# Performance work log

Measured on AMD Instinct MI355X. Metric: run time of the kernel, lower is better.

## Reference

```python
import jax, jax.numpy as jnp
import numpy as np

B, N, OBS, H, HEADS = 8192, 32, 128, 256, 4
HD = H // HEADS  # head dim = 64
GAIN = (0.125 / H) ** 0.5
LN_EPS = 1e-5


def _ln(x):
    # LayerNorm over last dim, no affine (elementwise_affine=False)
    m = x.mean(axis=-1, keepdims=True)
    v = ((x - m) ** 2).mean(axis=-1, keepdims=True)
    return (x - m) * jax.lax.rsqrt(v + LN_EPS)


def setup_inputs() -> dict:
    key = jax.random.key(0)
    ks = jax.random.split(key, 20)
    f32 = jnp.float32
    # weights stored (in, out) so y = x @ W + b (transpose of torch layout)
    def w(k, i, o, g):
        return (jax.random.normal(k, (i, o), dtype=f32) * g)
    inp = {
        "all_agent_obs": jax.random.normal(ks[0], (B, N, OBS), dtype=f32),
        # EntityEmbedding (obs-only): 1-layer LinearEncoder, normal init * t-fixup gain
        "W_emb": w(ks[1], OBS, H, GAIN), "b_emb": jnp.zeros((H,), f32),
        # ResidualSelfAttention projections
        "Wq": w(ks[2], H, H, GAIN), "bq": jnp.zeros((H,), f32),
        "Wk": w(ks[3], H, H, GAIN), "bk": jnp.zeros((H,), f32),
        "Wv": w(ks[4], H, H, GAIN), "bv": jnp.zeros((H,), f32),
        "Wo": w(ks[5], H, H, GAIN), "bo": jnp.zeros((H,), f32),
        # LinearEncoder tail (num_layers=2), kaiming-ish scale * t-fixup gain
        "W1": w(ks[6], H, H, GAIN), "b1": jnp.zeros((H,), f32),
        "W2": w(ks[7], H, H, GAIN), "b2": jnp.zeros((H,), f32),
        # value head: Linear(h_size + 1, 1)
        "Wval": w(ks[8], H + 1, 1, (1.0 / (H + 1)) ** 0.5), "bval": jnp.zeros((1,), f32),
    }
    return inp


def reference(all_agent_obs, W_emb, b_emb, Wq, bq, Wk, bk, Wv, bv, Wo, bo,
              W1, b1, W2, b2, Wval, bval):
    # --- EntityEmbedding: 1-layer MLP with SiLU ---
    ent = jax.nn.silu(jnp.einsum("bno,oh->bnh", all_agent_obs, W_emb) + b_emb)

    # --- ResidualSelfAttention (pre-norm, no mask) ---
    x = _ln(ent)                                        # embedding_norm
    q = (x @ Wq + bq).reshape(B, N, HEADS, HD)
    k = (x @ Wk + bk).reshape(B, N, HEADS, HD)
    v = (x @ Wv + bv).reshape(B, N, HEADS, HD)
    attn = jnp.einsum("bnhd,bmhd->bhnm", q, k) / jnp.sqrt(jnp.float32(HD))
    attn = jax.nn.softmax(attn, axis=-1)
    out = jnp.einsum("bhnm,bmhd->bnhd", attn, v).reshape(B, N, H)
    out = _ln(out @ Wo + bo + x)                        # fc_out + residual, residual_norm
    pooled = out.mean(axis=1)                           # (B, H) unmasked avg pool

    # --- LinearEncoder tail (2 layers, SiLU) ---
    enc = jax.nn.silu(pooled @ W1 + b1)
    enc = jax.nn.silu(enc @ W2 + b2)

    # --- norm agent count: max_agents updates to N, so val = N*2/N - 1 = 1.0 ---
    nc = jnp.ones((B, 1), dtype=enc.dtype)
    enc = jnp.concatenate([enc, nc], axis=-1)           # (B, H+1)
    return enc @ Wval + bval                            # (B, 1)
```

## Files before the change

### kernel.cpp

```cpp
#include <hip/hip_runtime.h>


typedef __bf16 bf16x8 __attribute__((ext_vector_type(8)));
typedef float f32x4 __attribute__((ext_vector_type(4)));
typedef unsigned short ushort_t;

#define DEVI static __device__ __forceinline__
#define MFMA16(a, b, cc) __builtin_amdgcn_mfma_f32_16x16x32_bf16((a), (b), (cc), 0, 0, 0)

#define WAITV2 asm volatile("s_waitcnt vmcnt(2)" ::: "memory")
#define WAITV0 asm volatile("s_waitcnt vmcnt(0)" ::: "memory")
#define WAITLG asm volatile("s_waitcnt lgkmcnt(0)" ::: "memory")
#define BAR() __builtin_amdgcn_s_barrier()

constexpr int OWemb_ = 0;
constexpr int OWq_   = 32768;
constexpr int OWk_   = OWq_ + 65536;
constexpr int OWv_   = OWk_ + 65536;
constexpr int OWo_   = OWv_ + 65536;
constexpr int OW1_   = OWo_ + 65536;
constexpr int OW2_   = OW1_ + 65536;

constexpr int OBS_STRIDE = 264;
constexpr int L_BST = 32768;
constexpr int L_PP  = 65536;
constexpr int LDS_TOTAL = 65536 + 2048;
static_assert(LDS_TOTAL <= 80 * 1024, "need <=80KB for 2 blocks/CU");

DEVI float silu_f(float x) { return x / (1.0f + __expf(-x)); }
DEVI f32x4 splat4(float x) { f32x4 v = {x, x, x, x}; return v; }
DEVI uint2 pack4(f32x4 v) {
  union { __bf16 h[4]; uint2 u; } x;
  x.h[0] = (__bf16)v[0]; x.h[1] = (__bf16)v[1];
  x.h[2] = (__bf16)v[2]; x.h[3] = (__bf16)v[3];
  return x.u;
}
DEVI f32x4 unpk(uint2 u) {
  union { uint2 u2; __bf16 h[4]; } x; x.u2 = u;
  f32x4 v = {(float)x.h[0], (float)x.h[1], (float)x.h[2], (float)x.h[3]};
  return v;
}
DEVI bf16x8 ld_frag(const char* p) { return *(const bf16x8*)p; }
DEVI bf16x8 u4b(unsigned a, unsigned b, unsigned cc, unsigned d) {
  union { unsigned u[4]; bf16x8 v; } x;
  x.u[0] = a; x.u[1] = b; x.u[2] = cc; x.u[3] = d;
  return x.v;
}
DEVI unsigned to_agpr(unsigned v) {
  unsigned d;
  asm volatile("v_accvgpr_write_b32 %0, %1" : "=a"(d) : "v"(v));
  return d;
}
DEVI unsigned from_agpr(unsigned a) {
  unsigned d;
  asm volatile("v_accvgpr_read_b32 %0, %1" : "=v"(d) : "a"(a));
  return d;
}
DEVI int xaddr(int row, int k4) {
  int t = row >> 4, cc = row & 15;
  int ks = k4 >> 5, kg = (k4 >> 3) & 3, half = (k4 >> 2) & 1;
  return ((t * 8 + ks) * 64 + kg * 16 + cc) * 16 + half * 8;
}

typedef const __attribute__((address_space(1))) unsigned int* gas_ptr;
typedef __attribute__((address_space(3))) unsigned int* las_ptr;
DEVI void gload16(const void* g, void* l) {
  __builtin_amdgcn_global_load_lds((gas_ptr)g, (las_ptr)l, 16, 0, 0);
}

constexpr int CSRC(int p) {
  return (p < 4)  ? (OWemb_ + p * 8192)
       : (p < 12) ? (OWq_ + (p - 4) * 8192)
       : (p < 20) ? (OWk_ + (p - 12) * 8192)
       : (p < 28) ? (OWv_ + (p - 20) * 8192)
                  : (OWo_ + (p - 28) * 8192);
}

DEVI void issue_chunk(const ushort_t* pw, int srcOff, char* bst, int slot, int wv, int lane) {
  char* dst = bst + slot * 16384 + wv * 2048;
  const ushort_t* s = pw + srcOff + wv * 1024 + (size_t)lane * 8;
  gload16(s, dst);
  gload16(s + 512, dst + 1024);
}
#define PH_ISSUE(p) issue_chunk(pw, CSRC(p), bst, (p) & 1, wv, lane)

__global__ void pack_weights(const float* __restrict__ Wemb, const float* __restrict__ Wq,
                             const float* __restrict__ Wk, const float* __restrict__ Wv,
                             const float* __restrict__ Wo, const float* __restrict__ W1,
                             const float* __restrict__ W2, ushort_t* __restrict__ ws) {
  int t = blockIdx.x * 256 + threadIdx.x;
  if (t >= 53248) return;
  const float* src;
  int dst, n, k0;
  if (t < 4096) {
    int rem = t & 1023;
    int ctg = rem >> 6, l = rem & 63;
    n = ctg * 16 + (l & 15);
    k0 = (t >> 10) * 32 + (l >> 4) * 8;
    src = Wemb; dst = OWemb_ + t * 8;
  } else if (t < 36864) {
    int u = t - 4096, m = u >> 13, loc = u & 8191;
    int rem = loc & 1023;
    int ctg = rem >> 6, l = rem & 63;
    n = ctg * 16 + (l & 15);
    k0 = (loc >> 10) * 32 + (l >> 4) * 8;
    src = (m == 0) ? Wq : (m == 1) ? Wk : (m == 2) ? Wv : Wo;
    dst = OWq_ + m * 65536 + loc * 8;
  } else {
    int u = t - 36864, m = u >> 13, loc = u & 8191;
    int ln = loc & 63, ks = (loc >> 6) & 7, ct = loc >> 9;
    n = ct * 16 + (ln & 15);
    k0 = ks * 32 + (ln >> 4) * 8;
    src = m ? W2 : W1; dst = OW1_ + m * 65536 + loc * 8;
  }
  union { __bf16 h[8]; uint4 u; } pk;
  #pragma unroll
  for (int j = 0; j < 8; ++j) pk.h[j] = (__bf16)src[(k0 + j) * 256 + n];
  *(uint4*)(ws + dst) = pk.u;
}

__global__ __launch_bounds__(512, 4)
void poca_fused(const float* __restrict__ obs, const ushort_t* __restrict__ pw,
                const float* __restrict__ b_emb, const float* __restrict__ bq,
                const float* __restrict__ bk, const float* __restrict__ bv,
                const float* __restrict__ bo, const float* __restrict__ b1,
                const float* __restrict__ b2, const float* __restrict__ Wval,
                const float* __restrict__ bval, float* __restrict__ out) {
  __shared__ __align__(128) char lds[LDS_TOTAL];
  const int tid = threadIdx.x;
  const int wv = tid >> 6, lane = tid & 63;
  const int g = lane >> 4, c = lane & 15;
  const int mg = wv >> 2, ng = wv & 3;
  char* xb = lds;
  char* bst = lds + L_BST;
  char* as_ = bst + wv * 4096;
  char* ppb = lds + L_PP;
  char* poolb = bst;
  char* y1b = bst + 8448;
  char* ptlb = bst + 16896;

  PH_ISSUE(0);

  {
    const float4* op = (const float4*)(obs + (size_t)blockIdx.x * 64 * 128);
    #pragma unroll
    for (int it = 0; it < 4; ++it) {
      int idx = it * 512 + tid;
      float4 v = op[idx];
      int row = idx >> 5, col4 = idx & 31;
      union { __bf16 h[4]; uint2 u; } cv;
      cv.h[0] = (__bf16)v.x; cv.h[1] = (__bf16)v.y;
      cv.h[2] = (__bf16)v.z; cv.h[3] = (__bf16)v.w;
      *(uint2*)(xb + row * OBS_STRIDE + col4 * 8) = cv.u;
    }
  }
  WAITLG;

  f32x4 acc[2][4];

  #pragma unroll
  for (int p = 0; p < 4; ++p) {
    PH_ISSUE(p + 1); WAITV2; BAR();
    if (p == 0) {
      #pragma unroll
      for (int ct = 0; ct < 4; ++ct) {
        f32x4 b_ = *(const f32x4*)(b_emb + ng * 64 + ct * 16 + g * 4);
        acc[0][ct] = b_; acc[1][ct] = b_;
      }
    }
    const char* ck = bst + (p & 1) * 16384;
    bf16x8 wf[4], xf[2];
    #pragma unroll
    for (int t = 0; t < 4; ++t) wf[t] = ld_frag(ck + ((ng * 4 + t) * 64 + lane) * 16);
    #pragma unroll
    for (int rt = 0; rt < 2; ++rt)
      xf[rt] = ld_frag(xb + ((mg * 2 + rt) * 16 + c) * OBS_STRIDE + p * 64 + g * 16);
    #pragma unroll
    for (int rt = 0; rt < 2; ++rt)
      #pragma unroll
      for (int ct = 0; ct < 4; ++ct) acc[rt][ct] = MFMA16(wf[ct], xf[rt], acc[rt][ct]);
    WAITLG; BAR();
  }

  #pragma unroll
  for (int rt = 0; rt < 2; ++rt)
    #pragma unroll
    for (int ct = 0; ct < 4; ++ct)
      #pragma unroll
      for (int r = 0; r < 4; ++r) acc[rt][ct][r] = silu_f(acc[rt][ct][r]);
  #pragma unroll
  for (int rt = 0; rt < 2; ++rt) {
    float s1 = 0.f, s2 = 0.f;
    #pragma unroll
    for (int ct = 0; ct < 4; ++ct)
      #pragma unroll
      for (int r = 0; r < 4; ++r) { float e = acc[rt][ct][r]; s1 += e; s2 += e * e; }
    s1 += __shfl_xor(s1, 16); s2 += __shfl_xor(s2, 16);
    s1 += __shfl_xor(s1, 32); s2 += __shfl_xor(s2, 32);
    if (g == 0)
      *(float2*)(ppb + (mg * 32 + rt * 16 + c) * 32 + ng * 8) = make_float2(s1, s2);
  }
  WAITLG; BAR();
  {
    float mu[2], rs[2];
    #pragma unroll
    for (int rt = 0; rt < 2; ++rt) {
      int row = mg * 32 + rt * 16 + c;
      f32x4 pA = *(const f32x4*)(ppb + row * 32);
      f32x4 pB = *(const f32x4*)(ppb + row * 32 + 16);
      float S1 = pA[0] + pA[2] + pB[0] + pB[2];
      float S2 = pA[1] + pA[3] + pB[1] + pB[3];
      float m_ = S1 * (1.f / 256.f);
      float v_ = S2 * (1.f / 256.f) - m_ * m_;
      mu[rt] = m_; rs[rt] = rsqrtf(v_ + 1e-5f);
    }
    #pragma unroll
    for (int rt = 0; rt < 2; ++rt)
      #pragma unroll
      for (int ct = 0; ct < 4; ++ct) {
        f32x4 xv;
        #pragma unroll
        for (int r = 0; r < 4; ++r) xv[r] = (acc[rt][ct][r] - mu[rt]) * rs[rt];
        *(uint2*)(xb + xaddr(mg * 32 + rt * 16 + c, ng * 64 + ct * 16 + g * 4)) = pack4(xv);
      }
  }
  WAITLG; BAR();

  #pragma unroll
  for (int p = 4; p < 12; ++p) {
    PH_ISSUE(p + 1); WAITV2; BAR();
    if (p == 4) {
      #pragma unroll
      for (int ct = 0; ct < 4; ++ct) {
        f32x4 b_ = *(const f32x4*)(bq + ng * 64 + ct * 16 + g * 4);
        acc[0][ct] = b_; acc[1][ct] = b_;
      }
    }
    const char* ck = bst + (p & 1) * 16384;
    const int ks = p - 4;
    bf16x8 wf[4], xf[2];
    #pragma unroll
    for (int t = 0; t < 4; ++t) wf[t] = ld_frag(ck + ((ng * 4 + t) * 64 + lane) * 16);
    #pragma unroll
    for (int rt = 0; rt < 2; ++rt)
      xf[rt] = ld_frag(xb + (((mg * 2 + rt) * 8 + ks) * 64 + lane) * 16);
    #pragma unroll
    for (int rt = 0; rt < 2; ++rt)
      #pragma unroll
      for (int ct = 0; ct < 4; ++ct) acc[rt][ct] = MFMA16(wf[ct], xf[rt], acc[rt][ct]);
    WAITLG; BAR();
  }

  unsigned qs[16];
  #pragma unroll
  for (int rt = 0; rt < 2; ++rt)
    #pragma unroll
    for (int ct = 0; ct < 4; ++ct) {
      uint2 qp = pack4(acc[rt][ct]);
      qs[(rt * 4 + ct) * 2] = to_agpr(qp.x);
      qs[(rt * 4 + ct) * 2 + 1] = to_agpr(qp.y);
    }

  #pragma unroll
  for (int p = 12; p < 20; ++p) {
    if (p < 19) { PH_ISSUE(p + 1); WAITV2; } else { WAITV0; }
    BAR();
    if (p == 12) {
      #pragma unroll
      for (int ct = 0; ct < 4; ++ct) {
        f32x4 b_ = *(const f32x4*)(bk + ng * 64 + ct * 16 + g * 4);
        acc[0][ct] = b_; acc[1][ct] = b_;
      }
    }
    const char* ck = bst + (p & 1) * 16384;
    const int ks = p - 12;
    bf16x8 wf[4], xf[2];
    #pragma unroll
    for (int t = 0; t < 4; ++t) wf[t] = ld_frag(ck + ((ng * 4 + t) * 64 + lane) * 16);
    #pragma unroll
    for (int rt = 0; rt < 2; ++rt)
      xf[rt] = ld_frag(xb + (((mg * 2 + rt) * 8 + ks) * 64 + lane) * 16);
    #pragma unroll
    for (int rt = 0; rt < 2; ++rt)
      #pragma unroll
      for (int ct = 0; ct < 4; ++ct) acc[rt][ct] = MFMA16(wf[ct], xf[rt], acc[rt][ct]);
    WAITLG; BAR();
  }

  float rinv[2];
  uint2 p_pk[2][2];
  {
    f32x4 sacc[2][2];
    sacc[0][0] = splat4(0.f); sacc[0][1] = splat4(0.f);
    sacc[1][0] = splat4(0.f); sacc[1][1] = splat4(0.f);
    #pragma unroll
    for (int hf = 0; hf < 2; ++hf) {
      #pragma unroll
      for (int rt2 = 0; rt2 < 2; ++rt2)
        #pragma unroll
        for (int ctl = 0; ctl < 2; ++ctl) {
          int qi = (rt2 * 4 + hf * 2 + ctl) * 2;
          *(uint2*)(as_ + (rt2 * 16 + c) * 64 + (ctl * 16 + g * 4) * 2) =
              make_uint2(from_agpr(qs[qi]), from_agpr(qs[qi + 1]));
          *(uint2*)(as_ + 2048 + (rt2 * 16 + c) * 64 + (ctl * 16 + g * 4) * 2) =
              pack4(acc[rt2][hf * 2 + ctl]);
        }
      WAITLG;
      bf16x8 qf[2], kf[2];
      #pragma unroll
      for (int t = 0; t < 2; ++t) {
        qf[t] = ld_frag(as_ + (t * 16 + c) * 64 + g * 16);
        kf[t] = ld_frag(as_ + 2048 + (t * 16 + c) * 64 + g * 16);
      }
      #pragma unroll
      for (int qt = 0; qt < 2; ++qt)
        #pragma unroll
        for (int kt = 0; kt < 2; ++kt)
          sacc[qt][kt] = MFMA16(kf[kt], qf[qt], sacc[qt][kt]);
    }
    #pragma unroll
    for (int qt = 0; qt < 2; ++qt) {
      float sc[2][4];
      float mx = -3e38f;
      #pragma unroll
      for (int kt = 0; kt < 2; ++kt)
        #pragma unroll
        for (int r = 0; r < 4; ++r) { sc[kt][r] = sacc[qt][kt][r] * 0.125f; mx = fmaxf(mx, sc[kt][r]); }
      mx = fmaxf(mx, __shfl_xor(mx, 16));
      mx = fmaxf(mx, __shfl_xor(mx, 32));
      float sm = 0.f;
      #pragma unroll
      for (int kt = 0; kt < 2; ++kt)
        #pragma unroll
        for (int r = 0; r < 4; ++r) { float e = __expf(sc[kt][r] - mx); sc[kt][r] = e; sm += e; }
      sm += __shfl_xor(sm, 16);
      sm += __shfl_xor(sm, 32);
      rinv[qt] = 1.0f / sm;
      #pragma unroll
      for (int kt = 0; kt < 2; ++kt) {
        f32x4 pv = {sc[kt][0], sc[kt][1], sc[kt][2], sc[kt][3]};
        p_pk[qt][kt] = pack4(pv);
      }
    }
  }
  WAITLG; BAR();
  PH_ISSUE(20);

  #pragma unroll
  for (int p = 20; p < 28; ++p) {
    if (p < 27) { PH_ISSUE(p + 1); WAITV2; } else { WAITV0; }
    BAR();
    if (p == 20) {
      #pragma unroll
      for (int ct = 0; ct < 4; ++ct) {
        f32x4 b_ = splat4(bv[ng * 64 + ct * 16 + c]);
        acc[0][ct] = b_; acc[1][ct] = b_;
      }
    }
    const char* ck = bst + (p & 1) * 16384;
    const int ks = p - 20;
    bf16x8 wf[4], xf[2];
    #pragma unroll
    for (int t = 0; t < 4; ++t) wf[t] = ld_frag(ck + ((ng * 4 + t) * 64 + lane) * 16);
    #pragma unroll
    for (int rt = 0; rt < 2; ++rt)
      xf[rt] = ld_frag(xb + (((mg * 2 + rt) * 8 + ks) * 64 + lane) * 16);
    #pragma unroll
    for (int rt = 0; rt < 2; ++rt)
      #pragma unroll
      for (int ct = 0; ct < 4; ++ct) acc[rt][ct] = MFMA16(xf[rt], wf[ct], acc[rt][ct]);
    WAITLG; BAR();
  }

  {
    uint2 respk[2][4];
    #pragma unroll
    for (int rt = 0; rt < 2; ++rt)
      #pragma unroll
      for (int ct = 0; ct < 4; ++ct)
        respk[rt][ct] = *(uint2*)(xb + xaddr(mg * 32 + rt * 16 + c, ng * 64 + ct * 16 + g * 4));
    #pragma unroll
    for (int rt2 = 0; rt2 < 2; ++rt2)
      #pragma unroll
      for (int ct = 0; ct < 4; ++ct)
        *(uint2*)(as_ + (ct * 16 + c) * 64 + (rt2 * 16 + g * 4) * 2) = pack4(acc[rt2][ct]);
    WAITLG;
    bf16x8 vf[4];
    #pragma unroll
    for (int dt = 0; dt < 4; ++dt) vf[dt] = ld_frag(as_ + (dt * 16 + c) * 64 + g * 16);
    const int l1 = (g & 1) * 32 + c, l2 = l1 + 16;
    const bool hi = (g >= 2);
    #pragma unroll
    for (int qt = 0; qt < 2; ++qt) {
      unsigned x0k0 = __shfl(p_pk[qt][0].x, l1), x0k1 = __shfl(p_pk[qt][1].x, l1);
      unsigned y0k0 = __shfl(p_pk[qt][0].y, l1), y0k1 = __shfl(p_pk[qt][1].y, l1);
      unsigned x1k0 = __shfl(p_pk[qt][0].x, l2), x1k1 = __shfl(p_pk[qt][1].x, l2);
      unsigned y1k0 = __shfl(p_pk[qt][0].y, l2), y1k1 = __shfl(p_pk[qt][1].y, l2);
      bf16x8 pf = u4b(hi ? x0k1 : x0k0, hi ? y0k1 : y0k0, hi ? x1k1 : x1k0, hi ? y1k1 : y1k0);
      #pragma unroll
      for (int dt = 0; dt < 4; ++dt) {
        f32x4 o = splat4(0.f);
        o = MFMA16(vf[dt], pf, o);
        #pragma unroll
        for (int r = 0; r < 4; ++r) o[r] *= rinv[qt];
        *(uint2*)(xb + xaddr(mg * 32 + qt * 16 + c, ng * 64 + dt * 16 + g * 4)) = pack4(o);
      }
    }
    #pragma unroll
    for (int ct = 0; ct < 4; ++ct) {
      f32x4 b_ = *(const f32x4*)(bo + ng * 64 + ct * 16 + g * 4);
      #pragma unroll
      for (int rt = 0; rt < 2; ++rt) acc[rt][ct] = b_ + unpk(respk[rt][ct]);
    }
  }
  WAITLG; BAR();
  PH_ISSUE(28);

  #pragma unroll
  for (int p = 28; p < 36; ++p) {
    if (p < 35) { PH_ISSUE(p + 1); WAITV2; } else { WAITV0; }
    BAR();
    const char* ck = bst + (p & 1) * 16384;
    const int ks = p - 28;
    bf16x8 wf[4], xf[2];
    #pragma unroll
    for (int t = 0; t < 4; ++t) wf[t] = ld_frag(ck + ((ng * 4 + t) * 64 + lane) * 16);
    #pragma unroll
    for (int rt = 0; rt < 2; ++rt)
      xf[rt] = ld_frag(xb + (((mg * 2 + rt) * 8 + ks) * 64 + lane) * 16);
    #pragma unroll
    for (int rt = 0; rt < 2; ++rt)
      #pragma unroll
      for (int ct = 0; ct < 4; ++ct) acc[rt][ct] = MFMA16(wf[ct], xf[rt], acc[rt][ct]);
    WAITLG; BAR();
  }

  #pragma unroll
  for (int rt = 0; rt < 2; ++rt) {
    float s1 = 0.f, s2 = 0.f;
    #pragma unroll
    for (int ct = 0; ct < 4; ++ct)
      #pragma unroll
      for (int r = 0; r < 4; ++r) { float e = acc[rt][ct][r]; s1 += e; s2 += e * e; }
    s1 += __shfl_xor(s1, 16); s2 += __shfl_xor(s2, 16);
    s1 += __shfl_xor(s1, 32); s2 += __shfl_xor(s2, 32);
    if (g == 0)
      *(float2*)(ppb + (mg * 32 + rt * 16 + c) * 32 + ng * 8) = make_float2(s1, s2);
  }
  WAITLG; BAR();
  {
    float mu[2], rs[2];
    #pragma unroll
    for (int rt = 0; rt < 2; ++rt) {
      int row = mg * 32 + rt * 16 + c;
      f32x4 pA = *(const f32x4*)(ppb + row * 32);
      f32x4 pB = *(const f32x4*)(ppb + row * 32 + 16);
      float S1 = pA[0] + pA[2] + pB[0] + pB[2];
      float S2 = pA[1] + pA[3] + pB[1] + pB[3];
      float m_ = S1 * (1.f / 256.f);
      float v_ = S2 * (1.f / 256.f) - m_ * m_;
      mu[rt] = m_; rs[rt] = rsqrtf(v_ + 1e-5f);
    }
    f32x4 ps[4];
    #pragma unroll
    for (int ct = 0; ct < 4; ++ct) {
      #pragma unroll
      for (int r = 0; r < 4; ++r)
        ps[ct][r] = (acc[0][ct][r] - mu[0]) * rs[0] + (acc[1][ct][r] - mu[1]) * rs[1];
    }
    #pragma unroll
    for (int st = 1; st < 16; st <<= 1)
      #pragma unroll
      for (int ct = 0; ct < 4; ++ct)
        #pragma unroll
        for (int r = 0; r < 4; ++r) ps[ct][r] += __shfl_xor(ps[ct][r], st);
    if (c == 0) {
      #pragma unroll
      for (int ct = 0; ct < 4; ++ct) {
        f32x4 pv;
        #pragma unroll
        for (int r = 0; r < 4; ++r) pv[r] = ps[ct][r] * (1.f / 32.f);
        *(uint2*)(poolb + mg * 528 + (ng * 64 + ct * 16 + g * 4) * 2) = pack4(pv);
      }
    }
  }
  #pragma unroll
  for (int it = 0; it < 4; ++it) {
    int idx = it * 512 + tid;
    if (idx < 1792) {
      int row = 2 + (idx >> 7), col = idx & 127;
      *(unsigned*)(poolb + row * 528 + col * 4) = 0;
      *(unsigned*)(y1b + row * 528 + col * 4) = 0;
    }
  }
  WAITLG; BAR();

  f32x4 t1[2];
  #pragma unroll
  for (int ctl = 0; ctl < 2; ++ctl) t1[ctl] = splat4(b1[wv * 32 + ctl * 16 + c]);
  #pragma unroll
  for (int ks = 0; ks < 8; ++ks) {
    bf16x8 a = ld_frag(poolb + c * 528 + ks * 64 + g * 16);
    #pragma unroll
    for (int ctl = 0; ctl < 2; ++ctl) {
      bf16x8 b = *(const bf16x8*)(pw + OW1_ + (size_t)(((wv * 2 + ctl) * 8 + ks) * 64 + lane) * 8);
      t1[ctl] = MFMA16(a, b, t1[ctl]);
    }
  }
  if (g == 0) {
    #pragma unroll
    for (int ctl = 0; ctl < 2; ++ctl)
      #pragma unroll
      for (int r = 0; r < 4; ++r)
        *(__bf16*)(y1b + r * 528 + (wv * 32 + ctl * 16 + c) * 2) = (__bf16)silu_f(t1[ctl][r]);
  }
  WAITLG; BAR();
  f32x4 t2[2];
  #pragma unroll
  for (int ctl = 0; ctl < 2; ++ctl) t2[ctl] = splat4(b2[wv * 32 + ctl * 16 + c]);
  #pragma unroll
  for (int ks = 0; ks < 8; ++ks) {
    bf16x8 a = ld_frag(y1b + c * 528 + ks * 64 + g * 16);
    #pragma unroll
    for (int ctl = 0; ctl < 2; ++ctl) {
      bf16x8 b = *(const bf16x8*)(pw + OW2_ + (size_t)(((wv * 2 + ctl) * 8 + ks) * 64 + lane) * 8);
      t2[ctl] = MFMA16(a, b, t2[ctl]);
    }
  }
  if (g == 0) {
    float part[4] = {0.f, 0.f, 0.f, 0.f};
    #pragma unroll
    for (int ctl = 0; ctl < 2; ++ctl) {
      float wvv = Wval[wv * 32 + ctl * 16 + c];
      #pragma unroll
      for (int r = 0; r < 4; ++r) part[r] += silu_f(t2[ctl][r]) * wvv;
    }
    #pragma unroll
    for (int m = 1; m < 16; m <<= 1) {
      #pragma unroll
      for (int r = 0; r < 4; ++r) part[r] += __shfl_xor(part[r], m);
    }
    if (c == 0) {
      float4 p4 = make_float4(part[0], part[1], part[2], part[3]);
      *(float4*)(ptlb + wv * 16) = p4;
    }
  }
  WAITLG; BAR();
  if (tid < 2) {
    float s = Wval[256] + bval[0];
    const float* pt = (const float*)ptlb;
    #pragma unroll
    for (int w8 = 0; w8 < 8; ++w8) s += pt[w8 * 4 + tid];
    out[(size_t)blockIdx.x * 2 + tid] = s;
  }
}

extern "C" void kernel_launch(void* const* d_in, const int* in_sizes, int n_in,
                              void* d_out, int out_size, void* d_ws, size_t ws_size,
                              hipStream_t stream) {
  (void)in_sizes; (void)n_in; (void)out_size; (void)ws_size;
  const float* obs  = (const float*)d_in[0];
  const float* Wemb = (const float*)d_in[1];
  const float* bemb = (const float*)d_in[2];
  const float* Wq   = (const float*)d_in[3];
  const float* bq   = (const float*)d_in[4];
  const float* Wk   = (const float*)d_in[5];
  const float* bk   = (const float*)d_in[6];
  const float* Wv   = (const float*)d_in[7];
  const float* bv   = (const float*)d_in[8];
  const float* Wo   = (const float*)d_in[9];
  const float* bo   = (const float*)d_in[10];
  const float* W1   = (const float*)d_in[11];
  const float* b1   = (const float*)d_in[12];
  const float* W2   = (const float*)d_in[13];
  const float* b2   = (const float*)d_in[14];
  const float* Wval = (const float*)d_in[15];
  const float* bval = (const float*)d_in[16];
  ushort_t* ws = (ushort_t*)d_ws;
  float* out = (float*)d_out;

  pack_weights<<<208, 256, 0, stream>>>(Wemb, Wq, Wk, Wv, Wo, W1, W2, ws);
  poca_fused<<<4096, 512, 0, stream>>>(obs, ws, bemb, bq, bk, bv, bo, b1, b2, Wval, bval, out);
}
```

Before: 328.9 us.

## Reorder V before K projection and swizzle LDS staging for attention fragments

Computes the V projection before K, parks packed V in AGPRs, then runs K so attention scores, softmax and PV follow without a pipeline break. The prefetch of the next weight chunk now continues straight through the phase boundary, removing the drain-and-reissue between phases. LDS staging of Q/K/V switches to a lane-contiguous layout so fragment reads are linear per lane, meant to reduce bank conflicts. In exchange it raises register pressure by holding both Q and V packed in AGPRs at once.

New measurement: 332.9 us. Within noise of the previous version (+1.2%).

```diff
diff --git a/kernel.cpp b/kernel.cpp
--- a/kernel.cpp
+++ b/kernel.cpp
@@ -71,8 +71,8 @@
 constexpr int CSRC(int p) {
   return (p < 4)  ? (OWemb_ + p * 8192)
        : (p < 12) ? (OWq_ + (p - 4) * 8192)
-       : (p < 20) ? (OWk_ + (p - 12) * 8192)
-       : (p < 28) ? (OWv_ + (p - 20) * 8192)
+       : (p < 20) ? (OWv_ + (p - 12) * 8192)
+       : (p < 28) ? (OWk_ + (p - 20) * 8192)
                   : (OWo_ + (p - 28) * 8192);
 }
 
@@ -263,12 +263,11 @@
 
   #pragma unroll
   for (int p = 12; p < 20; ++p) {
-    if (p < 19) { PH_ISSUE(p + 1); WAITV2; } else { WAITV0; }
-    BAR();
+    PH_ISSUE(p + 1); WAITV2; BAR();
     if (p == 12) {
       #pragma unroll
       for (int ct = 0; ct < 4; ++ct) {
-        f32x4 b_ = *(const f32x4*)(bk + ng * 64 + ct * 16 + g * 4);
+        f32x4 b_ = splat4(bv[ng * 64 + ct * 16 + c]);
         acc[0][ct] = b_; acc[1][ct] = b_;
       }
     }
@@ -283,12 +282,46 @@
     #pragma unroll
     for (int rt = 0; rt < 2; ++rt)
       #pragma unroll
+      for (int ct = 0; ct < 4; ++ct) acc[rt][ct] = MFMA16(xf[rt], wf[ct], acc[rt][ct]);
+    WAITLG; BAR();
+  }
+
+  unsigned vs[16];
+  #pragma unroll
+  for (int rt = 0; rt < 2; ++rt)
+    #pragma unroll
+    for (int ct = 0; ct < 4; ++ct) {
+      uint2 vp = pack4(acc[rt][ct]);
+      vs[(rt * 4 + ct) * 2] = to_agpr(vp.x);
+      vs[(rt * 4 + ct) * 2 + 1] = to_agpr(vp.y);
+    }
+
+  #pragma unroll
+  for (int p = 20; p < 28; ++p) {
+    if (p < 27) { PH_ISSUE(p + 1); WAITV2; } else { WAITV0; }
+    BAR();
+    if (p == 20) {
+      #pragma unroll
+      for (int ct = 0; ct < 4; ++ct) {
+        f32x4 b_ = *(const f32x4*)(bk + ng * 64 + ct * 16 + g * 4);
+        acc[0][ct] = b_; acc[1][ct] = b_;
+      }
+    }
+    const char* ck = bst + (p & 1) * 16384;
+    const int ks = p - 20;
+    bf16x8 wf[4], xf[2];
+    #pragma unroll
+    for (int t = 0; t < 4; ++t) wf[t] = ld_frag(ck + ((ng * 4 + t) * 64 + lane) * 16);
+    #pragma unroll
+    for (int rt = 0; rt < 2; ++rt)
+      xf[rt] = ld_frag(xb + (((mg * 2 + rt) * 8 + ks) * 64 + lane) * 16);
+    #pragma unroll
+    for (int rt = 0; rt < 2; ++rt)
+      #pragma unroll
       for (int ct = 0; ct < 4; ++ct) acc[rt][ct] = MFMA16(wf[ct], xf[rt], acc[rt][ct]);
     WAITLG; BAR();
   }
 
-  float rinv[2];
-  uint2 p_pk[2][2];
   {
     f32x4 sacc[2][2];
     sacc[0][0] = splat4(0.f); sacc[0][1] = splat4(0.f);
@@ -299,18 +332,18 @@
       for (int rt2 = 0; rt2 < 2; ++rt2)
         #pragma unroll
         for (int ctl = 0; ctl < 2; ++ctl) {
+          int gr = ctl * 2 + (g >> 1);
+          int off = rt2 * 1024 + (gr * 16 + c) * 16 + (g & 1) * 8;
           int qi = (rt2 * 4 + hf * 2 + ctl) * 2;
-          *(uint2*)(as_ + (rt2 * 16 + c) * 64 + (ctl * 16 + g * 4) * 2) =
-              make_uint2(from_agpr(qs[qi]), from_agpr(qs[qi + 1]));
-          *(uint2*)(as_ + 2048 + (rt2 * 16 + c) * 64 + (ctl * 16 + g * 4) * 2) =
-              pack4(acc[rt2][hf * 2 + ctl]);
+          *(uint2*)(as_ + off) = make_uint2(from_agpr(qs[qi]), from_agpr(qs[qi + 1]));
+          *(uint2*)(as_ + 2048 + off) = pack4(acc[rt2][hf * 2 + ctl]);
         }
       WAITLG;
       bf16x8 qf[2], kf[2];
       #pragma unroll
       for (int t = 0; t < 2; ++t) {
-        qf[t] = ld_frag(as_ + (t * 16 + c) * 64 + g * 16);
-        kf[t] = ld_frag(as_ + 2048 + (t * 16 + c) * 64 + g * 16);
+        qf[t] = ld_frag(as_ + t * 1024 + lane * 16);
+        kf[t] = ld_frag(as_ + 2048 + t * 1024 + lane * 16);
       }
       #pragma unroll
       for (int qt = 0; qt < 2; ++qt)
@@ -318,6 +351,8 @@
         for (int kt = 0; kt < 2; ++kt)
           sacc[qt][kt] = MFMA16(kf[kt], qf[qt], sacc[qt][kt]);
     }
+    float rinv[2];
+    uint2 p_pk[2][2];
     #pragma unroll
     for (int qt = 0; qt < 2; ++qt) {
       float sc[2][4];
@@ -342,52 +377,25 @@
         p_pk[qt][kt] = pack4(pv);
       }
     }
-  }
-  WAITLG; BAR();
-  PH_ISSUE(20);
-
-  #pragma unroll
-  for (int p = 20; p < 28; ++p) {
-    if (p < 27) { PH_ISSUE(p + 1); WAITV2; } else { WAITV0; }
-    BAR();
-    if (p == 20) {
-      #pragma unroll
-      for (int ct = 0; ct < 4; ++ct) {
-        f32x4 b_ = splat4(bv[ng * 64 + ct * 16 + c]);
-        acc[0][ct] = b_; acc[1][ct] = b_;
-      }
-    }
-    const char* ck = bst + (p & 1) * 16384;
-    const int ks = p - 20;
-    bf16x8 wf[4], xf[2];
-    #pragma unroll
-    for (int t = 0; t < 4; ++t) wf[t] = ld_frag(ck + ((ng * 4 + t) * 64 + lane) * 16);
-    #pragma unroll
-    for (int rt = 0; rt < 2; ++rt)
-      xf[rt] = ld_frag(xb + (((mg * 2 + rt) * 8 + ks) * 64 + lane) * 16);
-    #pragma unroll
-    for (int rt = 0; rt < 2; ++rt)
-      #pragma unroll
-      for (int ct = 0; ct < 4; ++ct) acc[rt][ct] = MFMA16(xf[rt], wf[ct], acc[rt][ct]);
-    WAITLG; BAR();
-  }
-
-  {
+    #pragma unroll
+    for (int rt2 = 0; rt2 < 2; ++rt2)
+      #pragma unroll
+      for (int ct = 0; ct < 4; ++ct) {
+        int gr = rt2 * 2 + (g >> 1);
+        int off = ct * 1024 + (gr * 16 + c) * 16 + (g & 1) * 8;
+        int vi = (rt2 * 4 + ct) * 2;
+        *(uint2*)(as_ + off) = make_uint2(from_agpr(vs[vi]), from_agpr(vs[vi + 1]));
+      }
     uint2 respk[2][4];
     #pragma unroll
     for (int rt = 0; rt < 2; ++rt)
       #pragma unroll
       for (int ct = 0; ct < 4; ++ct)
         respk[rt][ct] = *(uint2*)(xb + xaddr(mg * 32 + rt * 16 + c, ng * 64 + ct * 16 + g * 4));
-    #pragma unroll
-    for (int rt2 = 0; rt2 < 2; ++rt2)
-      #pragma unroll
-      for (int ct = 0; ct < 4; ++ct)
-        *(uint2*)(as_ + (ct * 16 + c) * 64 + (rt2 * 16 + g * 4) * 2) = pack4(acc[rt2][ct]);
     WAITLG;
     bf16x8 vf[4];
     #pragma unroll
-    for (int dt = 0; dt < 4; ++dt) vf[dt] = ld_frag(as_ + (dt * 16 + c) * 64 + g * 16);
+    for (int dt = 0; dt < 4; ++dt) vf[dt] = ld_frag(as_ + dt * 1024 + lane * 16);
     const int l1 = (g & 1) * 32 + c, l2 = l1 + 16;
     const bool hi = (g >= 2);
     #pragma unroll
```
